# Performance work log

Hardware: AMD Instinct MI355X
Metric: run time of the kernel (lower is better)

Reference implementation:

```python
import jax, jax.numpy as jnp
import numpy as np

B, L, M, F = 64, 1024, 256, 256


def setup_inputs() -> dict:
    key = jax.random.key(0)
    k1, k2 = jax.random.split(key)
    patch_features = jax.random.normal(k1, (B, L, F), dtype=jnp.float32)
    queue = jax.random.normal(k2, (L, M, F), dtype=jnp.float32)
    return {"patch_features": patch_features, "queue": queue}


def reference(patch_features, queue):
    # sim[b, l, m] = <patch_features[b, l], queue[l, m]>  (batched per-location matmul)
    sim = jnp.einsum('blf,lmf->blm', patch_features, queue)
    # original takes topk(5) then keeps only index 0 == argmax over memory slots
    idx = jnp.argmax(sim, axis=-1)                      # [B, L]
    # N[b, l] = queue[l, idx[b, l]]
    N = queue[jnp.arange(queue.shape[0])[None, :], idx]  # [B, L, F]
    return N
```

## Files before the change

### kernel.cpp

```cpp
#include <hip/hip_runtime.h>

#define B_ 64
#define L_ 1024
#define M_ 256
#define F_ 256

typedef __attribute__((ext_vector_type(8))) short short8;
typedef __attribute__((ext_vector_type(16))) float f32x16;
typedef unsigned int u32;

struct Frag3 { short8 h, m, l; };

__device__ __forceinline__ u32 asu(float f) { union { float f; u32 u; } c; c.f = f; return c.u; }
__device__ __forceinline__ float asf(u32 u) { union { float f; u32 u; } c; c.u = u; return c.f; }
__device__ __forceinline__ u32 pack2(u32 lo, u32 hi) {
    return __builtin_amdgcn_perm(hi, lo, 0x07060302u);
}
__device__ __forceinline__ float4 ld4(const float* p) {
    return *reinterpret_cast<const float4*>(p);
}

__device__ __forceinline__ void async_cp16(const float* g, float* l) {
    __builtin_amdgcn_global_load_lds(
        (const __attribute__((address_space(1))) u32*)g,
        (__attribute__((address_space(3))) u32*)l,
        16, 0, 0);
}

__device__ __forceinline__ Frag3 split8(float4 a, float4 b) {
    float x[8] = {a.x, a.y, a.z, a.w, b.x, b.y, b.z, b.w};
    u32 xb[8], rb[8], sb[8];
#pragma unroll
    for (int e = 0; e < 8; ++e) {
        xb[e] = asu(x[e]);
        float hf = asf(xb[e] & 0xFFFF0000u);
        float r  = x[e] - hf;
        rb[e] = asu(r);
        float mf = asf(rb[e] & 0xFFFF0000u);
        float r2 = r - mf;
        sb[e] = asu(r2);
    }
    union { u32 w[4]; short8 s; } H, M, Lo;
#pragma unroll
    for (int d = 0; d < 4; ++d) {
        H.w[d]  = pack2(xb[2 * d], xb[2 * d + 1]);
        M.w[d]  = pack2(rb[2 * d], rb[2 * d + 1]);
        Lo.w[d] = pack2(sb[2 * d], sb[2 * d + 1]);
    }
    Frag3 f; f.h = H.s; f.m = M.s; f.l = Lo.s; return f;
}

#define MFMA6(ACC, A, Bf)                                                        \
    ACC = __builtin_amdgcn_mfma_f32_32x32x16_bf16((A).m, (Bf).m, ACC, 0, 0, 0);  \
    ACC = __builtin_amdgcn_mfma_f32_32x32x16_bf16((A).h, (Bf).l, ACC, 0, 0, 0);  \
    ACC = __builtin_amdgcn_mfma_f32_32x32x16_bf16((A).l, (Bf).h, ACC, 0, 0, 0);  \
    ACC = __builtin_amdgcn_mfma_f32_32x32x16_bf16((A).h, (Bf).m, ACC, 0, 0, 0);  \
    ACC = __builtin_amdgcn_mfma_f32_32x32x16_bf16((A).m, (Bf).h, ACC, 0, 0, 0);  \
    ACC = __builtin_amdgcn_mfma_f32_32x32x16_bf16((A).h, (Bf).h, ACC, 0, 0, 0)

__launch_bounds__(256, 2)
__global__ void mq_mfma_lds_kernel(const float* __restrict__ patch,
                                   const float* __restrict__ queue,
                                   float* __restrict__ out) {
    const int l    = blockIdx.x;
    const int t    = threadIdx.x;
    const int lane = t & 63;
    const int w    = t >> 6;
    const int bt   = w & 1;
    const int mtg  = w >> 1;
    const int r32  = lane & 31;
    const int kh   = lane >> 5;

    __shared__ __align__(16) float Ql[2][256 * 32];
    __shared__ __align__(16) float Pl[2][64 * 32];

    const int lrow = lane >> 3;
    const int lcol = lane & 7;
    const float* qsrcw = queue + ((size_t)l * M_ + w * 64 + lrow) * F_ + (lcol ^ lrow) * 4;
    const float* psrcw = patch + ((size_t)(w * 16 + lrow) * L_ + l) * F_ + (lcol ^ lrow) * 4;

#define STAGE(FT, BUF)                                                            \
    {                                                                             \
        _Pragma("unroll")                                                         \
        for (int k = 0; k < 8; ++k)                                               \
            async_cp16(qsrcw + (size_t)k * 8 * F_ + (FT) * 32,                    \
                       &Ql[BUF][(w * 8 + k) * 256]);                              \
        _Pragma("unroll")                                                         \
        for (int k = 0; k < 2; ++k)                                               \
            async_cp16(psrcw + (size_t)k * 8 * L_ * F_ + (FT) * 32,               \
                       &Pl[BUF][(w * 2 + k) * 256]);                              \
    }

    f32x16 acc[4];
#pragma unroll
    for (int mt = 0; mt < 4; ++mt) acc[mt] = (f32x16)0.f;

    STAGE(0, 0);

    const int s7 = r32 & 7;
    const int ra = bt * 32 + r32;

#pragma unroll 1
    for (int ft = 0; ft < 8; ++ft) {
        __syncthreads();
        if (ft < 7) STAGE(ft + 1, (ft + 1) & 1);

        const float* Qb = Ql[ft & 1];
        const float* Pb = Pl[ft & 1];
#pragma unroll
        for (int kk = 0; kk < 2; ++kk) {
            const int c0 = kk * 4 + kh * 2;
            const float4 a0 = ld4(&Pb[ra * 32 + ((c0 ^ s7) * 4)]);
            const float4 a1 = ld4(&Pb[ra * 32 + (((c0 + 1) ^ s7) * 4)]);
            const Frag3 A = split8(a0, a1);
#pragma unroll
            for (int mt = 0; mt < 4; ++mt) {
                const int rb = mtg * 128 + mt * 32 + r32;
                const float4 b0 = ld4(&Qb[rb * 32 + ((c0 ^ s7) * 4)]);
                const float4 b1 = ld4(&Qb[rb * 32 + (((c0 + 1) ^ s7) * 4)]);
                const Frag3 Bf = split8(b0, b1);
                MFMA6(acc[mt], A, Bf);
            }
        }
    }

    float* pval = (float*)&Pl[0][0];
    int*   pidx = (int*)&Pl[0][0] + 128;
    int*   sidx = (int*)&Pl[0][0] + 256;
#pragma unroll
    for (int r = 0; r < 16; ++r) {
        float bv = acc[0][r];
        int   bi = mtg * 128 + r32;
#pragma unroll
        for (int mt = 1; mt < 4; ++mt) {
            const float cv = acc[mt][r];
            const int   ci = mtg * 128 + mt * 32 + r32;
            if (cv > bv) { bv = cv; bi = ci; }
        }
#pragma unroll
        for (int off = 16; off >= 1; off >>= 1) {
            const float ov = __shfl_xor(bv, off);
            const int   oi = __shfl_xor(bi, off);
            if (ov > bv || (ov == bv && oi < bi)) { bv = ov; bi = oi; }
        }
        if (r32 == 0) {
            const int b = bt * 32 + (r & 3) + 8 * (r >> 2) + 4 * kh;
            pval[mtg * 64 + b] = bv;
            pidx[mtg * 64 + b] = bi;
        }
    }
    __syncthreads();

    if (t < 64) {
        const float v0 = pval[t], v1 = pval[64 + t];
        sidx[t] = (v1 > v0) ? pidx[64 + t] : pidx[t];
    }
    __syncthreads();

    const int cb = t >> 6;
    const int cc = t & 63;
#pragma unroll
    for (int b0 = 0; b0 < 64; b0 += 4) {
        const int b  = b0 + cb;
        const int mi = sidx[b];
        const float4 v = ld4(&queue[((size_t)l * M_ + mi) * F_ + cc * 4]);
        *reinterpret_cast<float4*>(&out[((size_t)b * L_ + l) * F_ + cc * 4]) = v;
    }
}

extern "C" void kernel_launch(void* const* d_in, const int* in_sizes, int n_in,
                              void* d_out, int out_size, void* d_ws, size_t ws_size,
                              hipStream_t stream) {
    const float* patch = (const float*)d_in[0];
    const float* queue = (const float*)d_in[1];
    float* out = (float*)d_out;
    mq_mfma_lds_kernel<<<dim3(L_), dim3(256), 0, stream>>>(patch, queue, out);
}
```

Baseline: 106.7 us.

## Use 16-wave blocks with 4-stage async LDS pipeline and explicit vmcnt waits

```diff
diff --git a/kernel.cpp b/kernel.cpp
--- a/kernel.cpp
+++ b/kernel.cpp
@@ -58,10 +58,10 @@
     ACC = __builtin_amdgcn_mfma_f32_32x32x16_bf16((A).m, (Bf).h, ACC, 0, 0, 0);  \
     ACC = __builtin_amdgcn_mfma_f32_32x32x16_bf16((A).h, (Bf).h, ACC, 0, 0, 0)
 
-__launch_bounds__(256, 2)
-__global__ void mq_mfma_lds_kernel(const float* __restrict__ patch,
-                                   const float* __restrict__ queue,
-                                   float* __restrict__ out) {
+__launch_bounds__(1024)
+__global__ void mq_mfma_q4_kernel(const float* __restrict__ patch,
+                                  const float* __restrict__ queue,
+                                  float* __restrict__ out) {
     const int l    = blockIdx.x;
     const int t    = threadIdx.x;
     const int lane = t & 63;
@@ -70,73 +70,81 @@
     const int mtg  = w >> 1;
     const int r32  = lane & 31;
     const int kh   = lane >> 5;
+    const bool w8  = (w < 8);
 
-    __shared__ __align__(16) float Ql[2][256 * 32];
-    __shared__ __align__(16) float Pl[2][64 * 32];
+    __shared__ __align__(16) float Ql[4][256 * 32];
+    __shared__ __align__(16) float Pl[4][64 * 32];
 
     const int lrow = lane >> 3;
     const int lcol = lane & 7;
-    const float* qsrcw = queue + ((size_t)l * M_ + w * 64 + lrow) * F_ + (lcol ^ lrow) * 4;
-    const float* psrcw = patch + ((size_t)(w * 16 + lrow) * L_ + l) * F_ + (lcol ^ lrow) * 4;
+    const float* qsrcw = queue + ((size_t)l * M_ + w * 16 + lrow) * F_ + (lcol ^ lrow) * 4;
+    const float* psrcw = patch + ((size_t)((w & 7) * 8 + lrow) * L_ + l) * F_ + (lcol ^ lrow) * 4;
 
 #define STAGE(FT, BUF)                                                            \
     {                                                                             \
-        _Pragma("unroll")                                                         \
-        for (int k = 0; k < 8; ++k)                                               \
-            async_cp16(qsrcw + (size_t)k * 8 * F_ + (FT) * 32,                    \
-                       &Ql[BUF][(w * 8 + k) * 256]);                              \
-        _Pragma("unroll")                                                         \
-        for (int k = 0; k < 2; ++k)                                               \
-            async_cp16(psrcw + (size_t)k * 8 * L_ * F_ + (FT) * 32,               \
-                       &Pl[BUF][(w * 2 + k) * 256]);                              \
+        async_cp16(qsrcw + (FT) * 32, &Ql[BUF][(2 * w) * 256]);                   \
+        async_cp16(qsrcw + (size_t)8 * F_ + (FT) * 32, &Ql[BUF][(2 * w + 1) * 256]); \
+        if (w8) async_cp16(psrcw + (FT) * 32, &Pl[BUF][w * 256]);                 \
     }
 
-    f32x16 acc[4];
-#pragma unroll
-    for (int mt = 0; mt < 4; ++mt) acc[mt] = (f32x16)0.f;
+    f32x16 acc = (f32x16)0.f;
+
+    const int s7  = r32 & 7;
+    const int ra  = bt * 32 + r32;
+    const int rbm = mtg * 32 + r32;
+
+#define COMPUTE(FT)                                                               \
+    {                                                                             \
+        const float* Qb = &Ql[(FT) & 3][0];                                       \
+        const float* Pb = &Pl[(FT) & 3][0];                                       \
+        _Pragma("unroll")                                                         \
+        for (int kk = 0; kk < 2; ++kk) {                                          \
+            const int c0 = kk * 4 + kh * 2;                                       \
+            const float4 a0 = ld4(&Pb[ra * 32 + ((c0 ^ s7) * 4)]);                \
+            const float4 a1 = ld4(&Pb[ra * 32 + (((c0 + 1) ^ s7) * 4)]);          \
+            const Frag3 A = split8(a0, a1);                                       \
+            const float4 b0 = ld4(&Qb[rbm * 32 + ((c0 ^ s7) * 4)]);               \
+            const float4 b1 = ld4(&Qb[rbm * 32 + (((c0 + 1) ^ s7) * 4)]);         \
+            const Frag3 Bf = split8(b0, b1);                                      \
+            MFMA6(acc, A, Bf);                                                    \
+        }                                                                         \
+    }
+
+#define ITER(FT, V3, V2)                                                          \
+    {                                                                             \
+        __builtin_amdgcn_s_barrier();                                             \
+        __builtin_amdgcn_sched_barrier(0);                                        \
+        if ((FT) + 3 < 8) STAGE((FT) + 3, ((FT) + 3) & 3);                        \
+        if (w8) { asm volatile("s_waitcnt vmcnt(" #V3 ")" ::: "memory"); }        \
+        else    { asm volatile("s_waitcnt vmcnt(" #V2 ")" ::: "memory"); }        \
+        __builtin_amdgcn_sched_barrier(0);                                        \
+        __builtin_amdgcn_s_barrier();                                             \
+        __builtin_amdgcn_sched_barrier(0);                                        \
+        COMPUTE(FT);                                                              \
+    }
 
     STAGE(0, 0);
+    STAGE(1, 1);
+    STAGE(2, 2);
 
-    const int s7 = r32 & 7;
-    const int ra = bt * 32 + r32;
+    ITER(0, 9, 6);
+    ITER(1, 9, 6);
+    ITER(2, 9, 6);
+    ITER(3, 9, 6);
+    ITER(4, 9, 6);
+    ITER(5, 6, 4);
+    ITER(6, 3, 2);
+    ITER(7, 0, 0);
 
-#pragma unroll 1
-    for (int ft = 0; ft < 8; ++ft) {
-        __syncthreads();
-        if (ft < 7) STAGE(ft + 1, (ft + 1) & 1);
-
-        const float* Qb = Ql[ft & 1];
-        const float* Pb = Pl[ft & 1];
-#pragma unroll
-        for (int kk = 0; kk < 2; ++kk) {
-            const int c0 = kk * 4 + kh * 2;
-            const float4 a0 = ld4(&Pb[ra * 32 + ((c0 ^ s7) * 4)]);
-            const float4 a1 = ld4(&Pb[ra * 32 + (((c0 + 1) ^ s7) * 4)]);
-            const Frag3 A = split8(a0, a1);
-#pragma unroll
-            for (int mt = 0; mt < 4; ++mt) {
-                const int rb = mtg * 128 + mt * 32 + r32;
-                const float4 b0 = ld4(&Qb[rb * 32 + ((c0 ^ s7) * 4)]);
-                const float4 b1 = ld4(&Qb[rb * 32 + (((c0 + 1) ^ s7) * 4)]);
-                const Frag3 Bf = split8(b0, b1);
-                MFMA6(acc[mt], A, Bf);
-            }
-        }
-    }
+    __syncthreads();
 
     float* pval = (float*)&Pl[0][0];
-    int*   pidx = (int*)&Pl[0][0] + 128;
-    int*   sidx = (int*)&Pl[0][0] + 256;
+    int*   pidx = (int*)&Pl[0][0] + 512;
+    int*   sidx = (int*)&Pl[0][0] + 1024;
 #pragma unroll
     for (int r = 0; r < 16; ++r) {
-        float bv = acc[0][r];
-        int   bi = mtg * 128 + r32;
-#pragma unroll
-        for (int mt = 1; mt < 4; ++mt) {
-            const float cv = acc[mt][r];
-            const int   ci = mtg * 128 + mt * 32 + r32;
-            if (cv > bv) { bv = cv; bi = ci; }
-        }
+        float bv = acc[r];
+        int   bi = rbm;
 #pragma unroll
         for (int off = 16; off >= 1; off >>= 1) {
             const float ov = __shfl_xor(bv, off);
@@ -152,15 +160,21 @@
     __syncthreads();
 
     if (t < 64) {
-        const float v0 = pval[t], v1 = pval[64 + t];
-        sidx[t] = (v1 > v0) ? pidx[64 + t] : pidx[t];
+        float bv = pval[t];
+        int   bi = pidx[t];
+#pragma unroll
+        for (int g = 1; g < 8; ++g) {
+            const float cv = pval[g * 64 + t];
+            if (cv > bv) { bv = cv; bi = pidx[g * 64 + t]; }
+        }
+        sidx[t] = bi;
     }
     __syncthreads();
 
     const int cb = t >> 6;
     const int cc = t & 63;
 #pragma unroll
-    for (int b0 = 0; b0 < 64; b0 += 4) {
+    for (int b0 = 0; b0 < 64; b0 += 16) {
         const int b  = b0 + cb;
         const int mi = sidx[b];
         const float4 v = ld4(&queue[((size_t)l * M_ + mi) * F_ + cc * 4]);
@@ -174,5 +188,5 @@
     const float* patch = (const float*)d_in[0];
     const float* queue = (const float*)d_in[1];
     float* out = (float*)d_out;
-    mq_mfma_lds_kernel<<<dim3(L_), dim3(256), 0, stream>>>(patch, queue, out);
+    mq_mfma_q4_kernel<<<dim3(L_), dim3(1024), 0, stream>>>(patch, queue, out);
 }
```

After: 147.8 us. +38.5%, slower.
